# Kernel optimization log

Hardware: AMD Instinct MI355X
Metric: run time of the kernel (lower is better)

## Reference

```python
import jax, jax.numpy as jnp
import numpy as np

ALPHA = 0.4  # EMARecurrent(alpha=0.4, learnable=False); forward uses |alpha|


def setup_inputs() -> dict:
    key = jax.random.key(0)
    k1, _ = jax.random.split(key)
    inp = jax.random.normal(k1, (8, 1024, 4096), dtype=jnp.float32)  # [B, D, T]
    hidden = jnp.zeros((8, 1024, 1), dtype=jnp.float32)              # [B, D, 1]
    return {"inp": inp, "hidden": hidden}


def reference(inp, hidden):
    # hidden_t = |a| * x_t + (1 - |a|) * hidden_{t-1}, scanned over axis 2.
    a = jnp.abs(jnp.asarray(ALPHA, dtype=inp.dtype))
    xs = jnp.moveaxis(inp, 2, 0)          # [T, B, D]
    h0 = jnp.squeeze(hidden, axis=2)      # [B, D]

    def step(h, x):
        h = a * x + (1.0 - a) * h
        return h, h

    _, ys = jax.lax.scan(step, h0, xs)    # ys: [T, B, D]
    return jnp.moveaxis(ys, 0, 2)         # [B, D, T]
```

## Files before the change

kernel.cpp:

```cpp
#include <hip/hip_runtime.h>


constexpr int T_LEN = 4096;
constexpr int NT    = 16;

__global__ __launch_bounds__(256) void ema_wavescan2_kernel(
    const float* __restrict__ x,
    const float* __restrict__ h0,
    float* __restrict__ out,
    int nseq)
{
    const int gtid = blockIdx.x * blockDim.x + threadIdx.x;
    const int wave = gtid >> 6;
    const int lane = threadIdx.x & 63;
    if (wave >= nseq) return;

    const float a   = 0.4f;
    const float b   = 0.6f;
    const float b2  = b * b;
    const float b3  = b2 * b;
    const float b4  = b2 * b2;
    const float b8  = b4 * b4;
    const float b16 = b8 * b8;
    const float inv_b4 = 1.0f / b4;

    const float m1 = (lane >= 1) ? b4  : 0.0f;
    const float m2 = (lane >= 2) ? b8  : 0.0f;
    const float m3 = (lane >= 4) ? b16 : 0.0f;
    const float pb4i = exp2f((float)(4 * lane) * -0.73696559416f);

    const float4* __restrict__ xp = (const float4*)(x + (size_t)wave * T_LEN);
    float4* __restrict__ op       = (float4*)(out + (size_t)wave * T_LEN);

    float4 v[NT];
    #pragma unroll
    for (int it = 0; it < NT; ++it) v[it] = xp[it * 64 + lane];

    float h_in = h0[wave];

    #pragma unroll
    for (int it = 0; it < NT; ++it) {
        float4 w = v[it];

        float c0 = a * w.x;
        float c1 = fmaf(b, c0, a * w.y);
        float c2 = fmaf(b, c1, a * w.z);
        float c3 = fmaf(b, c2, a * w.w);

        float t = c3, u;
        u = __shfl_up(t, 1, 64); t = fmaf(m1, u, t);
        u = __shfl_up(t, 2, 64); t = fmaf(m2, u, t);
        u = __shfl_up(t, 4, 64); t = fmaf(m3, u, t);

        float e = fmaf(pb4i, h_in, (t - c3) * inv_b4);

        float4 o;
        o.x = fmaf(b , e, c0);
        o.y = fmaf(b2, e, c1);
        o.z = fmaf(b3, e, c2);
        o.w = fmaf(b4, e, c3);
        op[it * 64 + lane] = o;

        h_in = __shfl(t, 63, 64);
    }
}

extern "C" void kernel_launch(void* const* d_in, const int* in_sizes, int n_in,
                              void* d_out, int out_size, void* d_ws, size_t ws_size,
                              hipStream_t stream) {
    const float* x  = (const float*)d_in[0];
    const float* h0 = (const float*)d_in[1];
    float* out = (float*)d_out;

    const int nseq = in_sizes[1];
    const int block = 256;
    const int grid = (nseq * 64 + block - 1) / block;

    ema_wavescan2_kernel<<<grid, block, 0, stream>>>(x, h0, out, nseq);
}
```

Baseline: 231.1 us.

## Split each sequence into independent tiles with truncated warm-up carry

Each wave now handles one 256-element tile instead of a whole 4096-element sequence, which removes the serial chain of 16 carry steps. The incoming state for each tile is rebuilt by scanning the 32 preceding inputs (8 lanes of float4), relying on 0.6^32 decay so older history can be dropped. This raises wave-level parallelism and memory-level parallelism, at the cost of a small extra read per tile and a truncation error that is tiny but not exactly zero.

Measured after the change: 221.0 us. 1.05x faster.

```diff
diff --git a/kernel.cpp b/kernel.cpp
--- a/kernel.cpp
+++ b/kernel.cpp
@@ -1,19 +1,21 @@
 #include <hip/hip_runtime.h>
 
 
-constexpr int T_LEN = 4096;
-constexpr int NT    = 16;
+constexpr int TILES_PER_SEQ = 16;
 
-__global__ __launch_bounds__(256) void ema_wavescan2_kernel(
+__global__ __launch_bounds__(256) void ema_tile_kernel(
     const float* __restrict__ x,
     const float* __restrict__ h0,
     float* __restrict__ out,
-    int nseq)
+    int ntiles)
 {
     const int gtid = blockIdx.x * blockDim.x + threadIdx.x;
-    const int wave = gtid >> 6;
+    const int w    = gtid >> 6;
     const int lane = threadIdx.x & 63;
-    if (wave >= nseq) return;
+    if (w >= ntiles) return;
+
+    const int tidx = w & (TILES_PER_SEQ - 1);
+    const int seq  = w >> 4;
 
     const float a   = 0.4f;
     const float b   = 0.6f;
@@ -29,40 +31,52 @@
     const float m3 = (lane >= 4) ? b16 : 0.0f;
     const float pb4i = exp2f((float)(4 * lane) * -0.73696559416f);
 
-    const float4* __restrict__ xp = (const float4*)(x + (size_t)wave * T_LEN);
-    float4* __restrict__ op       = (float4*)(out + (size_t)wave * T_LEN);
+    const float4* __restrict__ xp = (const float4*)x;
+    float4* __restrict__ op       = (float4*)out;
 
-    float4 v[NT];
-    #pragma unroll
-    for (int it = 0; it < NT; ++it) v[it] = xp[it * 64 + lane];
+    const size_t tile_base = (size_t)w * 64;
 
-    float h_in = h0[wave];
+    float4 v = xp[tile_base + (size_t)lane];
 
-    #pragma unroll
-    for (int it = 0; it < NT; ++it) {
-        float4 w = v[it];
+    const bool has_warm = (tidx != 0);
+    float4 wv = make_float4(0.f, 0.f, 0.f, 0.f);
+    if (has_warm && lane < 8) {
+        wv = xp[tile_base - 8 + (size_t)lane];
+    }
 
-        float c0 = a * w.x;
-        float c1 = fmaf(b, c0, a * w.y);
-        float c2 = fmaf(b, c1, a * w.z);
-        float c3 = fmaf(b, c2, a * w.w);
+    float c0 = a * v.x;
+    float c1 = fmaf(b, c0, a * v.y);
+    float c2 = fmaf(b, c1, a * v.z);
+    float c3 = fmaf(b, c2, a * v.w);
 
-        float t = c3, u;
-        u = __shfl_up(t, 1, 64); t = fmaf(m1, u, t);
-        u = __shfl_up(t, 2, 64); t = fmaf(m2, u, t);
-        u = __shfl_up(t, 4, 64); t = fmaf(m3, u, t);
+    float t = c3, u;
+    u = __shfl_up(t, 1, 64); t = fmaf(m1, u, t);
+    u = __shfl_up(t, 2, 64); t = fmaf(m2, u, t);
+    u = __shfl_up(t, 4, 64); t = fmaf(m3, u, t);
 
-        float e = fmaf(pb4i, h_in, (t - c3) * inv_b4);
+    float h_in;
+    if (has_warm) {
+        float d0 = a * wv.x;
+        float d1 = fmaf(b, d0, a * wv.y);
+        float d2 = fmaf(b, d1, a * wv.z);
+        float d3 = fmaf(b, d2, a * wv.w);
+        float tw = d3;
+        u = __shfl_up(tw, 1, 64); tw = fmaf(m1, u, tw);
+        u = __shfl_up(tw, 2, 64); tw = fmaf(m2, u, tw);
+        u = __shfl_up(tw, 4, 64); tw = fmaf(m3, u, tw);
+        h_in = __shfl(tw, 7, 64);
+    } else {
+        h_in = h0[(size_t)seq];
+    }
 
-        float4 o;
-        o.x = fmaf(b , e, c0);
-        o.y = fmaf(b2, e, c1);
-        o.z = fmaf(b3, e, c2);
-        o.w = fmaf(b4, e, c3);
-        op[it * 64 + lane] = o;
+    float e = fmaf(pb4i, h_in, (t - c3) * inv_b4);
 
-        h_in = __shfl(t, 63, 64);
-    }
+    float4 o;
+    o.x = fmaf(b , e, c0);
+    o.y = fmaf(b2, e, c1);
+    o.z = fmaf(b3, e, c2);
+    o.w = fmaf(b4, e, c3);
+    op[tile_base + (size_t)lane] = o;
 }
 
 extern "C" void kernel_launch(void* const* d_in, const int* in_sizes, int n_in,
@@ -72,9 +86,11 @@
     const float* h0 = (const float*)d_in[1];
     float* out = (float*)d_out;
 
-    const int nseq = in_sizes[1];
-    const int block = 256;
-    const int grid = (nseq * 64 + block - 1) / block;
+    const int nseq   = in_sizes[1];
+    const int ntiles = nseq * TILES_PER_SEQ;
+    const int block  = 256;
+    const long long total = (long long)ntiles * 64;
+    const int grid = (int)((total + block - 1) / block);
 
-    ema_wavescan2_kernel<<<grid, block, 0, stream>>>(x, h0, out, nseq);
+    ema_tile_kernel<<<grid, block, 0, stream>>>(x, h0, out, ntiles);
 }
```
